# Kernel optimization log

Hardware: AMD Instinct MI355X
Metric: run time of the kernel (lower is better)

## Reference

```python
import jax, jax.numpy as jnp
import numpy as np

B, F = 512, 512
NUM_KERNEL, DIM_KERNEL = 50, 16


def setup_inputs() -> dict:
    key = jax.random.key(0)
    k1, k2 = jax.random.split(key)
    x = jax.random.normal(k1, (B, F), dtype=jnp.float32)
    # glorot-uniform-like scale for the learned kernel
    limit = (6.0 / (F + NUM_KERNEL * DIM_KERNEL)) ** 0.5
    W = jax.random.uniform(k2, (F, NUM_KERNEL * DIM_KERNEL), dtype=jnp.float32,
                           minval=-limit, maxval=limit)
    return {"x": x, "W": W}


def reference(x, W):
    # activation: (B, K, D)
    act = (x @ W).reshape(-1, NUM_KERNEL, DIM_KERNEL)
    # pairwise L1 over the kernel dim D: l1[b, b2, k] = sum_d |act[b,k,d] - act[b2,k,d]|
    diff = act[:, None, :, :] - act[None, :, :, :]      # (B, B, K, D)
    l1 = jnp.sum(jnp.abs(diff), axis=-1)                # (B, B, K)
    features = jnp.sum(jnp.exp(-l1), axis=1)            # (B, K), includes self-term (=1)
    return jnp.concatenate([x, features], axis=1)       # (B, F + K)
```

## Files before the change

### kernel.cpp

```cpp
#include <hip/hip_runtime.h>
#include <hip/hip_bf16.h>


#define B_ROWS 512
#define F_IN   512
#define NK     50
#define DK     16
#define N_COLS (NK * DK)
#define OUT_COLS (F_IN + NK)

#if __has_builtin(__builtin_amdgcn_exp2f)
#define EXP2F __builtin_amdgcn_exp2f
#else
#define EXP2F exp2f
#endif

typedef __attribute__((ext_vector_type(8))) short bf16x8;
typedef __attribute__((ext_vector_type(4))) float f32x4;

__device__ __forceinline__ short bfs(float f) {
    __hip_bfloat16 h = __float2bfloat16(f);
    return *reinterpret_cast<short*>(&h);
}

__global__ __launch_bounds__(64) void gemm_direct_kernel(const float* __restrict__ x,
                                                         const float* __restrict__ W,
                                                         float* __restrict__ act,
                                                         float* __restrict__ out) {
    const int l = threadIdx.x;
    const int mBase = blockIdx.x * 16;
    const int nBase = blockIdx.y * 32;
    const int rc = l & 15, kg = l >> 4;

    if (blockIdx.y == 0) {
        #pragma unroll
        for (int i = 0; i < 32; ++i) {
            int idx = l + i * 64;
            int r = idx >> 7, c4 = idx & 127;
            float4 v = *(const float4*)(x + (mBase + r) * F_IN + c4 * 4);
            float* o = out + (mBase + r) * OUT_COLS + c4 * 4;
            *(float2*)o = make_float2(v.x, v.y);
            *(float2*)(o + 2) = make_float2(v.z, v.w);
        }
    }

    const float* pa = x + (mBase + rc) * F_IN + kg * 8;
    const float* pb = W + (kg * 8) * N_COLS + nBase + rc;

    f32x4 acc0 = {0.f, 0.f, 0.f, 0.f};
    f32x4 acc1 = {0.f, 0.f, 0.f, 0.f};

    #pragma unroll
    for (int ks = 0; ks < 16; ++ks) {
        float4 a0 = *(const float4*)(pa + ks * 32);
        float4 a1 = *(const float4*)(pa + ks * 32 + 4);
        bf16x8 a;
        a[0] = bfs(a0.x); a[1] = bfs(a0.y); a[2] = bfs(a0.z); a[3] = bfs(a0.w);
        a[4] = bfs(a1.x); a[5] = bfs(a1.y); a[6] = bfs(a1.z); a[7] = bfs(a1.w);

        const float* pk = pb + (ks * 32) * N_COLS;
        bf16x8 b0, b1;
        #pragma unroll
        for (int j = 0; j < 8; ++j) {
            b0[j] = bfs(pk[j * N_COLS]);
            b1[j] = bfs(pk[j * N_COLS + 16]);
        }

        acc0 = __builtin_amdgcn_mfma_f32_16x16x32_bf16(a, b0, acc0, 0, 0, 0);
        acc1 = __builtin_amdgcn_mfma_f32_16x16x32_bf16(a, b1, acc1, 0, 0, 0);
    }

    #pragma unroll
    for (int r = 0; r < 4; ++r) {
        act[(mBase + kg * 4 + r) * N_COLS + nBase + rc]      = acc0[r];
        act[(mBase + kg * 4 + r) * N_COLS + nBase + 16 + rc] = acc1[r];
    }
}

__global__ __launch_bounds__(256) void pairwise_kernel(const float* __restrict__ act,
                                                       float* __restrict__ out) {
    const int k = blockIdx.x;
    const int chunk = blockIdx.y;
    __shared__ float4 Av[B_ROWS * 4];

    const int tid = threadIdx.x;
    const float* base = act + k * DK;
    #pragma unroll
    for (int i = 0; i < 8; ++i) {
        int idx = tid + i * 256;
        int b = idx >> 2, d4 = idx & 3;
        Av[idx ^ ((idx >> 6) & 7)] = *(const float4*)(base + b * N_COLS + d4 * 4);
    }
    __syncthreads();

    const int rt = tid >> 5;
    const int q = tid & 31;
    const int row0 = chunk * 32 + rt * 4;

    float4 m[4][4];
    #pragma unroll
    for (int r = 0; r < 4; ++r) {
        int gr = row0 + r;
        int xr = (gr >> 4) & 7;
        #pragma unroll
        for (int j = 0; j < 4; ++j)
            m[r][j] = Av[(gr * 4 + j) ^ xr];
    }

    const float4* bq = Av + q * 64;
    const int xm = q & 7;

    float acc[4] = {0.f, 0.f, 0.f, 0.f};
    #pragma unroll 4
    for (int i = 0; i < 16; ++i) {
        float4 v0 = bq[(i * 4 + 0) ^ xm];
        float4 v1 = bq[(i * 4 + 1) ^ xm];
        float4 v2 = bq[(i * 4 + 2) ^ xm];
        float4 v3 = bq[(i * 4 + 3) ^ xm];
        #pragma unroll
        for (int r = 0; r < 4; ++r) {
            float s0 = fabsf(m[r][0].x - v0.x) + fabsf(m[r][0].y - v0.y)
                     + fabsf(m[r][0].z - v0.z) + fabsf(m[r][0].w - v0.w);
            float s1 = fabsf(m[r][1].x - v1.x) + fabsf(m[r][1].y - v1.y)
                     + fabsf(m[r][1].z - v1.z) + fabsf(m[r][1].w - v1.w);
            float s2 = fabsf(m[r][2].x - v2.x) + fabsf(m[r][2].y - v2.y)
                     + fabsf(m[r][2].z - v2.z) + fabsf(m[r][2].w - v2.w);
            float s3 = fabsf(m[r][3].x - v3.x) + fabsf(m[r][3].y - v3.y)
                     + fabsf(m[r][3].z - v3.z) + fabsf(m[r][3].w - v3.w);
            float l1 = (s0 + s1) + (s2 + s3);
            acc[r] += EXP2F(l1 * -1.4426950408889634f);
        }
    }

    #pragma unroll
    for (int r = 0; r < 4; ++r) {
        acc[r] += __shfl_xor(acc[r], 1);
        acc[r] += __shfl_xor(acc[r], 2);
        acc[r] += __shfl_xor(acc[r], 4);
        acc[r] += __shfl_xor(acc[r], 8);
        acc[r] += __shfl_xor(acc[r], 16);
    }
    if (q == 0) {
        #pragma unroll
        for (int r = 0; r < 4; ++r)
            out[(row0 + r) * OUT_COLS + F_IN + k] = acc[r];
    }
}

extern "C" void kernel_launch(void* const* d_in, const int* in_sizes, int n_in,
                              void* d_out, int out_size, void* d_ws, size_t ws_size,
                              hipStream_t stream) {
    const float* x = (const float*)d_in[0];
    const float* W = (const float*)d_in[1];
    float* out = (float*)d_out;
    float* act = (float*)d_ws;

    gemm_direct_kernel<<<dim3(32, 25), dim3(64), 0, stream>>>(x, W, act, out);
    pairwise_kernel<<<dim3(50, 16), dim3(256), 0, stream>>>(act, out);
}
```

Measured before the change: 35.62 us.

## Split GEMM K across four waves and compute pairwise L1 in packed half2

The GEMM now runs four waves per block, each covering a quarter of the K dimension, and reduces their partial MFMA accumulators through shared memory before writing act. The x-to-out copy is spread over the first 128 blocks. The pairwise kernel stores activations as fp16 in LDS and computes the abs-diff sums with packed half2 arithmetic, halving LDS traffic and ALU ops. The cost is fp16 rounding of activations and partial sums, which could hurt accuracy. The split-K step adds a shared-memory reduction and a barrier.

```diff
diff --git a/kernel.cpp b/kernel.cpp
--- a/kernel.cpp
+++ b/kernel.cpp
@@ -1,5 +1,6 @@
 #include <hip/hip_runtime.h>
 #include <hip/hip_bf16.h>
+#include <hip/hip_fp16.h>
 
 
 #define B_ROWS 512
@@ -23,35 +24,40 @@
     return *reinterpret_cast<short*>(&h);
 }
 
-__global__ __launch_bounds__(64) void gemm_direct_kernel(const float* __restrict__ x,
-                                                         const float* __restrict__ W,
-                                                         float* __restrict__ act,
-                                                         float* __restrict__ out) {
-    const int l = threadIdx.x;
-    const int mBase = blockIdx.x * 16;
-    const int nBase = blockIdx.y * 32;
-    const int rc = l & 15, kg = l >> 4;
+__global__ __launch_bounds__(256) void gemm_ksplit_kernel(const float* __restrict__ x,
+                                                          const float* __restrict__ W,
+                                                          float* __restrict__ act,
+                                                          float* __restrict__ out) {
+    __shared__ float red[4 * 64 * 8];
 
-    if (blockIdx.y == 0) {
+    const int tid = threadIdx.x;
+    const int wave = tid >> 6, l = tid & 63;
+    const int bid = blockIdx.y * 32 + blockIdx.x;
+
+    if (bid < 128) {
         #pragma unroll
-        for (int i = 0; i < 32; ++i) {
-            int idx = l + i * 64;
-            int r = idx >> 7, c4 = idx & 127;
-            float4 v = *(const float4*)(x + (mBase + r) * F_IN + c4 * 4);
-            float* o = out + (mBase + r) * OUT_COLS + c4 * 4;
+        for (int i = 0; i < 2; ++i) {
+            int gid = bid * 512 + i * 256 + tid;
+            int row = gid >> 7, c4 = gid & 127;
+            float4 v = ((const float4*)x)[gid];
+            float* o = out + row * OUT_COLS + c4 * 4;
             *(float2*)o = make_float2(v.x, v.y);
             *(float2*)(o + 2) = make_float2(v.z, v.w);
         }
     }
 
-    const float* pa = x + (mBase + rc) * F_IN + kg * 8;
-    const float* pb = W + (kg * 8) * N_COLS + nBase + rc;
+    const int mBase = blockIdx.x * 16;
+    const int nBase = blockIdx.y * 32;
+    const int rc = l & 15, kg = l >> 4;
+
+    const float* pa = x + (mBase + rc) * F_IN + wave * 128 + kg * 8;
+    const float* pb = W + (wave * 128 + kg * 8) * N_COLS + nBase + rc;
 
     f32x4 acc0 = {0.f, 0.f, 0.f, 0.f};
     f32x4 acc1 = {0.f, 0.f, 0.f, 0.f};
 
     #pragma unroll
-    for (int ks = 0; ks < 16; ++ks) {
+    for (int ks = 0; ks < 4; ++ks) {
         float4 a0 = *(const float4*)(pa + ks * 32);
         float4 a1 = *(const float4*)(pa + ks * 32 + 4);
         bf16x8 a;
@@ -65,23 +71,36 @@
             b0[j] = bfs(pk[j * N_COLS]);
             b1[j] = bfs(pk[j * N_COLS + 16]);
         }
-
         acc0 = __builtin_amdgcn_mfma_f32_16x16x32_bf16(a, b0, acc0, 0, 0, 0);
         acc1 = __builtin_amdgcn_mfma_f32_16x16x32_bf16(a, b1, acc1, 0, 0, 0);
     }
 
-    #pragma unroll
-    for (int r = 0; r < 4; ++r) {
-        act[(mBase + kg * 4 + r) * N_COLS + nBase + rc]      = acc0[r];
-        act[(mBase + kg * 4 + r) * N_COLS + nBase + 16 + rc] = acc1[r];
+    const int ro = (wave * 64 + l) * 8;
+    *(f32x4*)(red + ro)     = acc0;
+    *(f32x4*)(red + ro + 4) = acc1;
+    __syncthreads();
+
+    {
+        const int e = tid * 2;
+        const int le = e >> 3, j0 = e & 7;
+        float2 s = make_float2(0.f, 0.f);
+        #pragma unroll
+        for (int w = 0; w < 4; ++w) {
+            float2 v = *(const float2*)(red + w * 512 + e);
+            s.x += v.x; s.y += v.y;
+        }
+        const int row = mBase + (le >> 4) * 4 + (j0 & 3);
+        const int col = nBase + (le & 15) + (j0 >> 2) * 16;
+        act[row * N_COLS + col]       = s.x;
+        act[(row + 1) * N_COLS + col] = s.y;
     }
 }
 
-__global__ __launch_bounds__(256) void pairwise_kernel(const float* __restrict__ act,
-                                                       float* __restrict__ out) {
+__global__ __launch_bounds__(256) void pairwise_h2_kernel(const float* __restrict__ act,
+                                                          float* __restrict__ out) {
     const int k = blockIdx.x;
     const int chunk = blockIdx.y;
-    __shared__ float4 Av[B_ROWS * 4];
+    __shared__ uint2 Ah4[B_ROWS * 4];
 
     const int tid = threadIdx.x;
     const float* base = act + k * DK;
@@ -89,7 +108,13 @@
     for (int i = 0; i < 8; ++i) {
         int idx = tid + i * 256;
         int b = idx >> 2, d4 = idx & 3;
-        Av[idx ^ ((idx >> 6) & 7)] = *(const float4*)(base + b * N_COLS + d4 * 4);
+        float4 v = *(const float4*)(base + b * N_COLS + d4 * 4);
+        __half2 h0 = __float22half2_rn(make_float2(v.x, v.y));
+        __half2 h1 = __float22half2_rn(make_float2(v.z, v.w));
+        uint2 u;
+        u.x = __builtin_bit_cast(unsigned, h0);
+        u.y = __builtin_bit_cast(unsigned, h1);
+        Ah4[idx ^ ((idx >> 6) & 15)] = u;
     }
     __syncthreads();
 
@@ -97,38 +122,40 @@
     const int q = tid & 31;
     const int row0 = chunk * 32 + rt * 4;
 
-    float4 m[4][4];
+    __half2 m[4][8];
     #pragma unroll
     for (int r = 0; r < 4; ++r) {
         int gr = row0 + r;
-        int xr = (gr >> 4) & 7;
+        int xr = (gr >> 4) & 15;
         #pragma unroll
-        for (int j = 0; j < 4; ++j)
-            m[r][j] = Av[(gr * 4 + j) ^ xr];
+        for (int j = 0; j < 4; ++j) {
+            uint2 u = Ah4[(gr * 4 + j) ^ xr];
+            m[r][2 * j]     = __builtin_bit_cast(__half2, u.x);
+            m[r][2 * j + 1] = __builtin_bit_cast(__half2, u.y);
+        }
     }
 
-    const float4* bq = Av + q * 64;
-    const int xm = q & 7;
+    const uint2* bq = Ah4 + q * 64;
+    const int xm = q & 15;
 
     float acc[4] = {0.f, 0.f, 0.f, 0.f};
     #pragma unroll 4
     for (int i = 0; i < 16; ++i) {
-        float4 v0 = bq[(i * 4 + 0) ^ xm];
-        float4 v1 = bq[(i * 4 + 1) ^ xm];
-        float4 v2 = bq[(i * 4 + 2) ^ xm];
-        float4 v3 = bq[(i * 4 + 3) ^ xm];
+        __half2 v[8];
+        #pragma unroll
+        for (int j = 0; j < 4; ++j) {
+            uint2 u = bq[(i * 4 + j) ^ xm];
+            v[2 * j]     = __builtin_bit_cast(__half2, u.x);
+            v[2 * j + 1] = __builtin_bit_cast(__half2, u.y);
+        }
         #pragma unroll
         for (int r = 0; r < 4; ++r) {
-            float s0 = fabsf(m[r][0].x - v0.x) + fabsf(m[r][0].y - v0.y)
-                     + fabsf(m[r][0].z - v0.z) + fabsf(m[r][0].w - v0.w);
-            float s1 = fabsf(m[r][1].x - v1.x) + fabsf(m[r][1].y - v1.y)
-                     + fabsf(m[r][1].z - v1.z) + fabsf(m[r][1].w - v1.w);
-            float s2 = fabsf(m[r][2].x - v2.x) + fabsf(m[r][2].y - v2.y)
-                     + fabsf(m[r][2].z - v2.z) + fabsf(m[r][2].w - v2.w);
-            float s3 = fabsf(m[r][3].x - v3.x) + fabsf(m[r][3].y - v3.y)
-                     + fabsf(m[r][3].z - v3.z) + fabsf(m[r][3].w - v3.w);
-            float l1 = (s0 + s1) + (s2 + s3);
-            acc[r] += EXP2F(l1 * -1.4426950408889634f);
+            __half2 s = __habs2(__hsub2(m[r][0], v[0]));
+            #pragma unroll
+            for (int jj = 1; jj < 8; ++jj)
+                s = __hadd2(s, __habs2(__hsub2(m[r][jj], v[jj])));
+            float2 f = __half22float2(s);
+            acc[r] += EXP2F((f.x + f.y) * -1.4426950408889634f);
         }
     }
 
@@ -155,6 +182,6 @@
     float* out = (float*)d_out;
     float* act = (float*)d_ws;
 
-    gemm_direct_kernel<<<dim3(32, 25), dim3(64), 0, stream>>>(x, W, act, out);
-    pairwise_kernel<<<dim3(50, 16), dim3(256), 0, stream>>>(act, out);
+    gemm_ksplit_kernel<<<dim3(32, 25), dim3(256), 0, stream>>>(x, W, act, out);
+    pairwise_h2_kernel<<<dim3(50, 16), dim3(256), 0, stream>>>(act, out);
 }
```

Measured after the change: 32.05 us. -10.0%, faster.
